# Performance work log

Hardware: AMD Instinct MI355X
Metric: run time of the kernel (lower is better)

The kernel has to match this reference:

```python
import jax, jax.numpy as jnp
import numpy as np

SEQ, BATCH, HID, NLAYERS = 2048, 16, 1024, 2


def setup_inputs() -> dict:
    key = jax.random.key(0)
    ks = jax.random.split(key, 3)
    scale = 1.0 / np.sqrt(HID)
    x = jax.random.normal(ks[0], (SEQ, BATCH, HID), dtype=jnp.float32)
    W0 = jax.random.normal(ks[1], (HID, 3 * HID), dtype=jnp.float32) * scale
    b0 = jnp.zeros((2 * HID,), dtype=jnp.float32)
    W1 = jax.random.normal(ks[2], (HID, 3 * HID), dtype=jnp.float32) * scale
    b1 = jnp.zeros((2 * HID,), dtype=jnp.float32)
    return {"x": x, "W0": W0, "b0": b0, "W1": W1, "b1": b1}


def _sru_layer(x, W, b):
    # x: [L, B, H]; W: [H, 3H]; b: [2H]
    L, B, H = x.shape
    U = jnp.einsum('lbd,dk->lbk', x, W)  # [L, B, 3H]
    x_tilde = U[..., :H]
    bf, br = b[:H], b[H:]
    f = jax.nn.sigmoid(U[..., H:2 * H] + bf)  # forget gate [L,B,H]
    r = jax.nn.sigmoid(U[..., 2 * H:] + br)   # reset gate  [L,B,H]

    def step(c_prev, inp):
        xt_t, f_t = inp
        c_t = f_t * c_prev + (1.0 - f_t) * xt_t
        return c_t, c_t

    c0 = jnp.zeros((B, H), dtype=x.dtype)
    _, cs = jax.lax.scan(step, c0, (x_tilde, f))  # cs: [L, B, H]
    h = r * cs + (1.0 - r) * x  # highway connection
    return h


def reference(x, W0, b0, W1, b1):
    h = _sru_layer(x, W0, b0)
    h = _sru_layer(h, W1, b1)
    return h[-1:]  # [1, B, H], matching `out[-1:]`
```

## Files before the change

kernel.cpp:

```cpp
#include <hip/hip_runtime.h>

#define SEQ    2048
#define BATCH  16
#define HID    1024
#define M_TOT  (SEQ*BATCH)
#define NCH    (BATCH*HID)
#define NCHUNK 64
#define TCHUNK (SEQ/NCHUNK)
#define NSEG   256

typedef __attribute__((ext_vector_type(8))) short          short8;
typedef __attribute__((ext_vector_type(8))) unsigned short ushort8_t;
typedef __attribute__((ext_vector_type(4))) float          floatx4;

__device__ __forceinline__ unsigned short f32_to_bf16(float f) {
  unsigned int u = __float_as_uint(f);
  u += 0x7FFFu + ((u >> 16) & 1u);
  return (unsigned short)(u >> 16);
}
__device__ __forceinline__ float bf16_to_f32(unsigned short h) {
  return __uint_as_float(((unsigned int)h) << 16);
}
__device__ __forceinline__ float sigmoidf_(float x) {
  return 1.f / (1.f + __expf(-x));
}


__device__ __forceinline__ void cast_swizzle_body(const float* __restrict__ src,
    unsigned short* __restrict__ dst, int mt, int kt, int t) {
  __shared__ unsigned short tile[4096];
  const int r = t >> 1, kh = (t & 1) * 16;
  const float* sp = src + (size_t)(mt * 128 + r) * 1024 + kt * 32 + kh;
  float4 v0 = *(const float4*)(sp + 0);
  float4 v1 = *(const float4*)(sp + 4);
  float4 v2 = *(const float4*)(sp + 8);
  float4 v3 = *(const float4*)(sp + 12);
  ushort8_t u0, u1;
  u0[0]=f32_to_bf16(v0.x); u0[1]=f32_to_bf16(v0.y); u0[2]=f32_to_bf16(v0.z); u0[3]=f32_to_bf16(v0.w);
  u0[4]=f32_to_bf16(v1.x); u0[5]=f32_to_bf16(v1.y); u0[6]=f32_to_bf16(v1.z); u0[7]=f32_to_bf16(v1.w);
  u1[0]=f32_to_bf16(v2.x); u1[1]=f32_to_bf16(v2.y); u1[2]=f32_to_bf16(v2.z); u1[3]=f32_to_bf16(v2.w);
  u1[4]=f32_to_bf16(v3.x); u1[5]=f32_to_bf16(v3.y); u1[6]=f32_to_bf16(v3.z); u1[7]=f32_to_bf16(v3.w);
  const int c = r >> 4, lr = r & 15, q0 = kh >> 3;
  const int unit0 = c * 64 + (q0 << 4) + lr;
  *(ushort8_t*)&tile[unit0 * 8]        = u0;
  *(ushort8_t*)&tile[(unit0 + 16) * 8] = u1;
  __syncthreads();
  const size_t base = ((size_t)mt * 32 + kt) * 4096;
  *(ushort8_t*)&dst[base + t * 16]     = *(const ushort8_t*)&tile[t * 16];
  *(ushort8_t*)&dst[base + t * 16 + 8] = *(const ushort8_t*)&tile[t * 16 + 8];
}

__device__ __forceinline__ void w_prep_body(const float* __restrict__ W,
    unsigned short* __restrict__ Wsw, int nt, int kt, int t) {
  __shared__ unsigned short tile[4096];
  const int kk = t >> 3, n0 = (t & 7) * 16;
  const float* sp = W + (size_t)(kt * 32 + kk) * 3072 + nt * 128 + n0;
  float v[16];
#pragma unroll
  for (int i = 0; i < 16; i += 4) {
    float4 f = *(const float4*)(sp + i);
    v[i] = f.x; v[i+1] = f.y; v[i+2] = f.z; v[i+3] = f.w;
  }
  const int cbase = (n0 >> 4) * 64 + ((kk >> 3) << 4);
#pragma unroll
  for (int j = 0; j < 16; j++)
    tile[(cbase + j) * 8 + (kk & 7)] = f32_to_bf16(v[j]);
  __syncthreads();
  const size_t base = ((size_t)nt * 32 + kt) * 4096;
  *(ushort8_t*)&Wsw[base + t * 16]     = *(const ushort8_t*)&tile[t * 16];
  *(ushort8_t*)&Wsw[base + t * 16 + 8] = *(const ushort8_t*)&tile[t * 16 + 8];
}

__global__ __launch_bounds__(256) void prep_all(const float* __restrict__ x,
    const float* __restrict__ W0, const float* __restrict__ W1,
    unsigned short* __restrict__ xsw, unsigned short* __restrict__ W0sw,
    unsigned short* __restrict__ W1sw) {
  const int id = blockIdx.x, t = threadIdx.x;
  if (id < 8192)        cast_swizzle_body(x, xsw, id >> 5, id & 31, t);
  else if (id < 8960)   w_prep_body(W0, W0sw, (id - 8192) >> 5, (id - 8192) & 31, t);
  else                  w_prep_body(W1, W1sw, (id - 8960) >> 5, (id - 8960) & 31, t);
}

__global__ __launch_bounds__(256, 2) void gemm_direct(
    const unsigned short* __restrict__ A, const unsigned short* __restrict__ B,
    unsigned short* __restrict__ Xt, unsigned short* __restrict__ Fo, unsigned short* __restrict__ Ro,
    const float* __restrict__ bias, int NBN2)
{
  const int tid = threadIdx.x;
  const int wave = tid >> 6, lane = tid & 63;
  const int wm = wave & 1, wn = wave >> 1;
  const int id = blockIdx.x;
  const int xcd = id & 7, slot = id >> 3;
  const int NB8 = NBN2 << 3;
  const int g = slot / NB8, rem = slot - g * NB8;
  const int bn = rem >> 3;
  const int bm = xcd * 32 + g * 8 + (rem & 7);

  const unsigned short* gA = A + (size_t)bm * 32 * 4096 + wm * 2048 + lane * 8;
  const unsigned short* gB = B + ((size_t)(bn * 2 + wn)) * 32 * 4096 + lane * 8;

  floatx4 acc[4][8];
#pragma unroll
  for (int i = 0; i < 4; i++)
#pragma unroll
    for (int j = 0; j < 8; j++)
#pragma unroll
      for (int r = 0; r < 4; r++) acc[i][j][r] = 0.f;

  short8 a0[4], b0[8], a1[4], b1[8];
  auto loadA = [&](short8* d, const unsigned short* p) {
#pragma unroll
    for (int i = 0; i < 4; i++) d[i] = *(const short8*)(p + i * 512);
  };
  auto loadB = [&](short8* d, const unsigned short* p) {
#pragma unroll
    for (int j = 0; j < 8; j++) d[j] = *(const short8*)(p + j * 512);
  };
  auto domfma = [&](short8* a, short8* b) {
#pragma unroll
    for (int i = 0; i < 4; i++)
#pragma unroll
      for (int j = 0; j < 8; j++)
        acc[i][j] = __builtin_amdgcn_mfma_f32_16x16x32_bf16(a[i], b[j], acc[i][j], 0, 0, 0);
  };

  loadA(a0, gA); loadB(b0, gB);
#pragma unroll 1
  for (int kt = 0; kt < 32; kt += 2) {
    loadA(a1, gA + 4096); loadB(b1, gB + 4096);
    domfma(a0, b0);
    gA += 8192; gB += 8192;
    if (kt + 2 < 32) { loadA(a0, gA); loadB(b0, gB); }
    domfma(a1, b1);
  }

  const int region = bn >> 2;
  const int lc = (bn & 3) * 256 + wn * 128 + (lane & 15);
  const int row0 = bm * 128 + wm * 64 + ((lane >> 4) << 2);
  if (region == 0) {
#pragma unroll
    for (int i = 0; i < 4; i++)
#pragma unroll
      for (int j = 0; j < 8; j++)
#pragma unroll
        for (int rg = 0; rg < 4; rg++)
          Xt[(size_t)(row0 + i * 16 + rg) * 1024 + lc + j * 16] = f32_to_bf16(acc[i][j][rg]);
  } else {
    unsigned short* O = (region == 1) ? Fo : Ro;
    const float* bp = bias + (region - 1) * 1024;
#pragma unroll
    for (int j = 0; j < 8; j++) {
      float bb = bp[lc + j * 16];
#pragma unroll
      for (int i = 0; i < 4; i++)
#pragma unroll
        for (int rg = 0; rg < 4; rg++) {
          float s = sigmoidf_(acc[i][j][rg] + bb);
          O[(size_t)(row0 + i * 16 + rg) * 1024 + lc + j * 16] = f32_to_bf16(s);
        }
    }
  }
}

__global__ __launch_bounds__(256, 2) void gemm2_scan(
    const unsigned short* __restrict__ A, const unsigned short* __restrict__ B,
    const float* __restrict__ bias, float* __restrict__ Pseg, float* __restrict__ Sseg)
{
  __shared__ float lps[2][64][4][4][2];
  const int tid = threadIdx.x;
  const int wave = tid >> 6, lane = tid & 63;
  const int wm = wave & 1, wn = wave >> 1;
  const int id = blockIdx.x;
  const int xcd = id & 7, slot = id >> 3;
  const int g = slot >> 6, rem = slot & 63;
  const int bn = rem >> 3;
  const int bm = xcd * 32 + g * 8 + (rem & 7);

  const unsigned short* gA  = A + (size_t)bm * 32 * 4096 + wm * 2048 + lane * 8;
  const unsigned short* gBx = B + (size_t)bn * 32 * 4096 + wn * 2048 + lane * 8;
  const unsigned short* gBf = B + (size_t)(8 + bn) * 32 * 4096 + wn * 2048 + lane * 8;

  floatx4 ax[4][4], af[4][4];
#pragma unroll
  for (int i = 0; i < 4; i++)
#pragma unroll
    for (int j = 0; j < 4; j++)
#pragma unroll
      for (int r = 0; r < 4; r++) { ax[i][j][r] = 0.f; af[i][j][r] = 0.f; }

  short8 a0[4], bx0[4], bf0[4], a1[4], bx1[4], bf1[4];
  auto load4 = [&](short8* d, const unsigned short* p) {
#pragma unroll
    for (int i = 0; i < 4; i++) d[i] = *(const short8*)(p + i * 512);
  };
  auto domfma = [&](short8* a, short8* bx, short8* bf) {
#pragma unroll
    for (int i = 0; i < 4; i++)
#pragma unroll
      for (int j = 0; j < 4; j++) {
        ax[i][j] = __builtin_amdgcn_mfma_f32_16x16x32_bf16(a[i], bx[j], ax[i][j], 0, 0, 0);
        af[i][j] = __builtin_amdgcn_mfma_f32_16x16x32_bf16(a[i], bf[j], af[i][j], 0, 0, 0);
      }
  };

  load4(a0, gA); load4(bx0, gBx); load4(bf0, gBf);
#pragma unroll 1
  for (int kt = 0; kt < 32; kt += 2) {
    load4(a1, gA + 4096); load4(bx1, gBx + 4096); load4(bf1, gBf + 4096);
    domfma(a0, bx0, bf0);
    gA += 8192; gBx += 8192; gBf += 8192;
    if (kt + 2 < 32) { load4(a0, gA); load4(bx0, gBx); load4(bf0, gBf); }
    domfma(a1, bx1, bf1);
  }

  const int q = lane >> 4, cc = lane & 15;
  float pv[4][4], sv[4][4];
#pragma unroll
  for (int j = 0; j < 4; j++) {
    float bb = bias[bn * 128 + wn * 64 + j * 16 + cc];
#pragma unroll
    for (int rg = 0; rg < 4; rg++) {
      float p = 1.f, s = 0.f;
#pragma unroll
      for (int i = 0; i < 4; i++) {
        float f  = sigmoidf_(af[i][j][rg] + bb);
        float xt = ax[i][j][rg];
        s = f * s + (1.f - f) * xt;
        p *= f;
      }
      pv[j][rg] = p; sv[j][rg] = s;
    }
  }
  if (wm == 0) {
#pragma unroll
    for (int j = 0; j < 4; j++)
#pragma unroll
      for (int rg = 0; rg < 4; rg++) {
        lps[wn][lane][rg][j][0] = pv[j][rg];
        lps[wn][lane][rg][j][1] = sv[j][rg];
      }
  }
  __syncthreads();
  if (wm == 1) {
#pragma unroll
    for (int j = 0; j < 4; j++) {
      const int h = bn * 128 + wn * 64 + j * 16 + cc;
#pragma unroll
      for (int rg = 0; rg < 4; rg++) {
        float plo = lps[wn][lane][rg][j][0];
        float slo = lps[wn][lane][rg][j][1];
        float phi = pv[j][rg], shi = sv[j][rg];
        const size_t off = (size_t)bm * NCH + (q * 4 + rg) * 1024 + h;
        Pseg[off] = plo * phi;
        Sseg[off] = phi * slo + shi;
      }
    }
  }
}

__global__ __launch_bounds__(256) void scan_pass1(
    const unsigned short* __restrict__ Xt, const unsigned short* __restrict__ F,
    float* __restrict__ P, float* __restrict__ S) {
  const int ch = (blockIdx.x * 256 + threadIdx.x) * 8;
  const int chunk = blockIdx.y;
  size_t idx = (size_t)chunk * TCHUNK * NCH + ch;
  float p[8], s[8];
#pragma unroll
  for (int j = 0; j < 8; j++) { p[j] = 1.f; s[j] = 0.f; }
  for (int t = 0; t < TCHUNK; ++t) {
    ushort8_t fv = *(const ushort8_t*)&F[idx];
    ushort8_t xv = *(const ushort8_t*)&Xt[idx];
#pragma unroll
    for (int j = 0; j < 8; j++) {
      float f  = bf16_to_f32(fv[j]);
      float xt = bf16_to_f32(xv[j]);
      s[j] = f * s[j] + (1.f - f) * xt;
      p[j] *= f;
    }
    idx += NCH;
  }
  float4* P4 = (float4*)&P[(size_t)chunk * NCH + ch];
  float4* S4 = (float4*)&S[(size_t)chunk * NCH + ch];
  P4[0] = make_float4(p[0], p[1], p[2], p[3]);
  P4[1] = make_float4(p[4], p[5], p[6], p[7]);
  S4[0] = make_float4(s[0], s[1], s[2], s[3]);
  S4[1] = make_float4(s[4], s[5], s[6], s[7]);
}

__global__ __launch_bounds__(256) void combine_c0(
    const float* __restrict__ P, const float* __restrict__ S, float* __restrict__ C0) {
  const int ch = blockIdx.x * 256 + threadIdx.x;
  float c = 0.f;
#pragma unroll 4
  for (int k = 0; k < NCHUNK; ++k) {
    C0[(size_t)k * NCH + ch] = c;
    c = P[(size_t)k * NCH + ch] * c + S[(size_t)k * NCH + ch];
  }
}

#define TPAD 4112
__global__ __launch_bounds__(256) void scan1_pass2_fused(
    const unsigned short* __restrict__ Xt, const unsigned short* __restrict__ F,
    const unsigned short* __restrict__ R, unsigned short* __restrict__ xsw,
    const float* __restrict__ C0, unsigned short* __restrict__ h1last)
{
  __shared__ unsigned short st[4 * TPAD];
  const int hb = blockIdx.x;
  const int chunk = blockIdx.y;
  const int tid = threadIdx.x;
  const int b = tid >> 4, hg = tid & 15;
  const int h0 = hb * 128 + hg * 8;
  const int ch = b * 1024 + h0;
  const int tl   = hg >> 2;
  const int usub = (hg & 3) * 16 + b;

  float c[8];
  {
    const float4* C4 = (const float4*)&C0[(size_t)chunk * NCH + ch];
    float4 a = C4[0], d = C4[1];
    c[0]=a.x; c[1]=a.y; c[2]=a.z; c[3]=a.w; c[4]=d.x; c[5]=d.y; c[6]=d.z; c[7]=d.w;
  }

  size_t idx = (size_t)chunk * TCHUNK * NCH + ch;
  for (int t8 = 0; t8 < TCHUNK / 8; ++t8) {
#pragma unroll
    for (int ts = 0; ts < 8; ++ts) {
      const int t = chunk * TCHUNK + t8 * 8 + ts;
      ushort8_t fv = *(const ushort8_t*)&F[idx];
      ushort8_t xv = *(const ushort8_t*)&Xt[idx];
      ushort8_t rv = *(const ushort8_t*)&R[idx];
      const size_t soff = ((size_t)(t >> 3) * 32 + (h0 >> 5)) * 4096
                        + (size_t)(((t & 7) * 64 + usub) * 8);
      ushort8_t xo = *(const ushort8_t*)&xsw[soff];
      ushort8_t hv;
#pragma unroll
      for (int j = 0; j < 8; ++j) {
        float f  = bf16_to_f32(fv[j]);
        float xt = bf16_to_f32(xv[j]);
        c[j] = f * c[j] + (1.f - f) * xt;
        float r  = bf16_to_f32(rv[j]);
        float xval = bf16_to_f32(xo[j]);
        hv[j] = f32_to_bf16(r * c[j] + (1.f - r) * xval);
      }
      *(ushort8_t*)&st[tl * TPAD + (ts * 64 + usub) * 8] = hv;
      if (t == SEQ - 1) *(ushort8_t*)&h1last[ch] = hv;
      idx += NCH;
    }
    __syncthreads();
    const size_t gbase = (((size_t)chunk * (TCHUNK / 8) + t8) * 32 + hb * 4) * 4096;
#pragma unroll
    for (int tl2 = 0; tl2 < 4; ++tl2) {
      size_t gdst = gbase + (size_t)tl2 * 4096 + tid * 16;
      *(ushort8_t*)&xsw[gdst]     = *(const ushort8_t*)&st[tl2 * TPAD + tid * 16];
      *(ushort8_t*)&xsw[gdst + 8] = *(const ushort8_t*)&st[tl2 * TPAD + tid * 16 + 8];
    }
    __syncthreads();
  }
}

__global__ __launch_bounds__(256) void r2_kernel(
    const unsigned short* __restrict__ h1last, const float* __restrict__ W1,
    const float* __restrict__ b1, float* __restrict__ r2) {
  __shared__ float xrow[1024];
  const int b = blockIdx.x, nq = blockIdx.y, tid = threadIdx.x;
  for (int i = tid; i < 1024; i += 256)
    xrow[i] = bf16_to_f32(h1last[b * 1024 + i]);
  __syncthreads();
  const int n = nq * 256 + tid;
  float acc = b1[1024 + n];
  for (int d = 0; d < 1024; ++d)
    acc += xrow[d] * W1[(size_t)d * 3072 + 2048 + n];
  r2[b * 1024 + n] = sigmoidf_(acc);
}

__global__ __launch_bounds__(256) void final_l2(
    const float* __restrict__ Pseg, const float* __restrict__ Sseg,
    const float* __restrict__ r2, const unsigned short* __restrict__ h1last,
    float* __restrict__ out) {
  const int ch = blockIdx.x * 256 + threadIdx.x;
  float c = 0.f;
#pragma unroll 8
  for (int k = 0; k < NSEG; ++k)
    c = Pseg[(size_t)k * NCH + ch] * c + Sseg[(size_t)k * NCH + ch];
  float r = r2[ch];
  float x = bf16_to_f32(h1last[ch]);
  out[ch] = r * c + (1.f - r) * x;
}

extern "C" void kernel_launch(void* const* d_in, const int* in_sizes, int n_in,
                              void* d_out, int out_size, void* d_ws, size_t ws_size,
                              hipStream_t stream) {
  const float* x  = (const float*)d_in[0];
  const float* W0 = (const float*)d_in[1];
  const float* b0 = (const float*)d_in[2];
  const float* W1 = (const float*)d_in[3];
  const float* b1 = (const float*)d_in[4];
  float* out = (float*)d_out;

  char* ws = (char*)d_ws;
  auto alloc = [&](size_t bytes) {
    char* p = ws; ws += (bytes + 255) & ~(size_t)255; return p;
  };
  const size_t NE = (size_t)M_TOT * HID;
  unsigned short* xsw   = (unsigned short*)alloc(NE * 2);
  unsigned short* W0sw  = (unsigned short*)alloc((size_t)3072 * 1024 * 2);
  unsigned short* W1sw  = (unsigned short*)alloc((size_t)3072 * 1024 * 2);
  unsigned short* Xt    = (unsigned short*)alloc(NE * 2);
  unsigned short* F     = (unsigned short*)alloc(NE * 2);
  unsigned short* R     = (unsigned short*)alloc(NE * 2);
  unsigned short* h1last= (unsigned short*)alloc((size_t)NCH * 2);
  float* P    = (float*)alloc((size_t)NCHUNK * NCH * 4);
  float* S    = (float*)alloc((size_t)NCHUNK * NCH * 4);
  float* C0   = (float*)alloc((size_t)NCHUNK * NCH * 4);
  float* Pseg = (float*)alloc((size_t)NSEG * NCH * 4);
  float* Sseg = (float*)alloc((size_t)NSEG * NCH * 4);
  float* r2   = (float*)alloc((size_t)NCH * 4);

  dim3 blk256(256);
  prep_all<<<dim3(9728), blk256, 0, stream>>>(x, W0, W1, xsw, W0sw, W1sw);
  gemm_direct<<<dim3(256 * 12), blk256, 0, stream>>>(xsw, W0sw, Xt, F, R, b0, 12);
  scan_pass1<<<dim3(8, NCHUNK), blk256, 0, stream>>>(Xt, F, P, S);
  combine_c0<<<dim3(NCH / 256), blk256, 0, stream>>>(P, S, C0);
  scan1_pass2_fused<<<dim3(8, NCHUNK), blk256, 0, stream>>>(Xt, F, R, xsw, C0, h1last);
  r2_kernel<<<dim3(16, 4), blk256, 0, stream>>>(h1last, W1, b1, r2);
  gemm2_scan<<<dim3(2048), blk256, 0, stream>>>(xsw, W1sw, b1, Pseg, Sseg);
  final_l2<<<dim3(NCH / 256), blk256, 0, stream>>>(Pseg, Sseg, r2, h1last, out);
}
```

Baseline: 757.9 us.

## Replace first-layer direct-load GEMM with LDS-staged 4-buffer pipelined GEMM

The first-layer projection GEMM used to feed MFMAs straight from global memory into registers. It now uses a 512-thread block computing a 256x256 tile. Operands are staged into a 4-slot LDS ring buffer via global_load_lds, and the A/B loads for stage t+3 are interleaved with the MFMA work of stage t, coordinated with barriers, setprio and partial vmcnt waits. This aims to raise reuse per loaded byte and hide global latency. The cost is 128KB of LDS per block, which limits residency to one block per CU, plus a more fragile hand-scheduled synchronisation scheme.

```diff
diff --git a/kernel.cpp b/kernel.cpp
--- a/kernel.cpp
+++ b/kernel.cpp
@@ -81,82 +81,157 @@
   else                  w_prep_body(W1, W1sw, (id - 8960) >> 5, (id - 8960) & 31, t);
 }
 
-__global__ __launch_bounds__(256, 2) void gemm_direct(
+typedef __attribute__((address_space(1))) const unsigned int GUI;
+typedef __attribute__((address_space(3))) unsigned int LUI;
+__device__ __forceinline__ void gl16(const unsigned short* g, unsigned short* l) {
+  __builtin_amdgcn_global_load_lds((GUI*)g, (LUI*)l, 16, 0, 0);
+}
+
+__global__ __launch_bounds__(512, 2) void gemm_pipe(
     const unsigned short* __restrict__ A, const unsigned short* __restrict__ B,
-    unsigned short* __restrict__ Xt, unsigned short* __restrict__ Fo, unsigned short* __restrict__ Ro,
-    const float* __restrict__ bias, int NBN2)
+    unsigned short* __restrict__ Xt, unsigned short* __restrict__ Fo,
+    unsigned short* __restrict__ Ro, const float* __restrict__ bias)
 {
+  __shared__ unsigned short lds[65536];
   const int tid = threadIdx.x;
   const int wave = tid >> 6, lane = tid & 63;
-  const int wm = wave & 1, wn = wave >> 1;
+  const int wm = wave >> 2, wn = wave & 3;
   const int id = blockIdx.x;
   const int xcd = id & 7, slot = id >> 3;
-  const int NB8 = NBN2 << 3;
-  const int g = slot / NB8, rem = slot - g * NB8;
-  const int bn = rem >> 3;
-  const int bm = xcd * 32 + g * 8 + (rem & 7);
-
-  const unsigned short* gA = A + (size_t)bm * 32 * 4096 + wm * 2048 + lane * 8;
-  const unsigned short* gB = B + ((size_t)(bn * 2 + wn)) * 32 * 4096 + lane * 8;
-
-  floatx4 acc[4][8];
-#pragma unroll
-  for (int i = 0; i < 4; i++)
-#pragma unroll
-    for (int j = 0; j < 8; j++)
-#pragma unroll
-      for (int r = 0; r < 4; r++) acc[i][j][r] = 0.f;
-
-  short8 a0[4], b0[8], a1[4], b1[8];
-  auto loadA = [&](short8* d, const unsigned short* p) {
-#pragma unroll
-    for (int i = 0; i < 4; i++) d[i] = *(const short8*)(p + i * 512);
-  };
-  auto loadB = [&](short8* d, const unsigned short* p) {
-#pragma unroll
-    for (int j = 0; j < 8; j++) d[j] = *(const short8*)(p + j * 512);
-  };
-  auto domfma = [&](short8* a, short8* b) {
-#pragma unroll
-    for (int i = 0; i < 4; i++)
-#pragma unroll
-      for (int j = 0; j < 8; j++)
-        acc[i][j] = __builtin_amdgcn_mfma_f32_16x16x32_bf16(a[i], b[j], acc[i][j], 0, 0, 0);
-  };
-
-  loadA(a0, gA); loadB(b0, gB);
+  const int g = slot / 96, r = slot % 96;
+  const int bn = r >> 3;
+  const int bm = xcd * 16 + g * 8 + (r & 7);
+
+  const unsigned short* aSrc0 = A + ((size_t)(2 * bm + 0) * 32) * 4096 + tid * 8;
+  const unsigned short* aSrc1 = A + ((size_t)(2 * bm + 1) * 32) * 4096 + tid * 8;
+  const unsigned short* bSrc0 = B + ((size_t)(2 * bn + 0) * 32) * 4096 + tid * 8;
+  const unsigned short* bSrc1 = B + ((size_t)(2 * bn + 1) * 32) * 4096 + tid * 8;
+
+  floatx4 acc[8][4];
+#pragma unroll
+  for (int i = 0; i < 8; i++)
+#pragma unroll
+    for (int j = 0; j < 4; j++)
+#pragma unroll
+      for (int rr = 0; rr < 4; rr++) acc[i][j][rr] = 0.f;
+
+#pragma unroll
+  for (int u = 0; u < 3; ++u) {
+    unsigned short* d = &lds[u * 16384 + wave * 512];
+    gl16(aSrc0 + (size_t)u * 4096, d);
+    gl16(aSrc1 + (size_t)u * 4096, d + 4096);
+    gl16(bSrc0 + (size_t)u * 4096, d + 8192);
+    gl16(bSrc1 + (size_t)u * 4096, d + 12288);
+  }
+  asm volatile("s_waitcnt vmcnt(0)" ::: "memory");
+  __builtin_amdgcn_s_barrier();
+
+  const int aoff = wm * 4096 + lane * 8;
+  const int boff = 8192 + (wn >> 1) * 4096 + (wn & 1) * 2048 + lane * 8;
+
 #pragma unroll 1
-  for (int kt = 0; kt < 32; kt += 2) {
-    loadA(a1, gA + 4096); loadB(b1, gB + 4096);
-    domfma(a0, b0);
-    gA += 8192; gB += 8192;
-    if (kt + 2 < 32) { loadA(a0, gA); loadB(b0, gB); }
-    domfma(a1, b1);
+  for (int t = 0; t < 29; ++t) {
+    __builtin_amdgcn_sched_barrier(0);
+    const int sb = (t & 3) * 16384;
+    const int u = t + 3;
+    const unsigned short* As = &lds[sb + aoff];
+    const unsigned short* Bs = &lds[sb + boff];
+    short8 br[4], ar[4];
+#pragma unroll
+    for (int nj = 0; nj < 4; ++nj) br[nj] = *(const short8*)(Bs + nj * 512);
+#pragma unroll
+    for (int mi = 0; mi < 4; ++mi) ar[mi] = *(const short8*)(As + mi * 512);
+    {
+      unsigned short* d = &lds[(u & 3) * 16384 + wave * 512];
+      gl16(aSrc0 + (size_t)u * 4096, d);
+      gl16(aSrc1 + (size_t)u * 4096, d + 4096);
+    }
+    __builtin_amdgcn_s_barrier();
+    __builtin_amdgcn_s_setprio(1);
+#pragma unroll
+    for (int mi = 0; mi < 4; ++mi)
+#pragma unroll
+      for (int nj = 0; nj < 4; ++nj)
+        acc[mi][nj] = __builtin_amdgcn_mfma_f32_16x16x32_bf16(ar[mi], br[nj], acc[mi][nj], 0, 0, 0);
+    __builtin_amdgcn_s_setprio(0);
+    __builtin_amdgcn_s_barrier();
+#pragma unroll
+    for (int mi = 0; mi < 4; ++mi) ar[mi] = *(const short8*)(As + (4 + mi) * 512);
+    {
+      unsigned short* d = &lds[(u & 3) * 16384 + 8192 + wave * 512];
+      gl16(bSrc0 + (size_t)u * 4096, d);
+      gl16(bSrc1 + (size_t)u * 4096, d + 4096);
+    }
+    __builtin_amdgcn_s_barrier();
+    __builtin_amdgcn_s_setprio(1);
+#pragma unroll
+    for (int mi = 0; mi < 4; ++mi)
+#pragma unroll
+      for (int nj = 0; nj < 4; ++nj)
+        acc[4 + mi][nj] = __builtin_amdgcn_mfma_f32_16x16x32_bf16(ar[mi], br[nj], acc[4 + mi][nj], 0, 0, 0);
+    __builtin_amdgcn_s_setprio(0);
+    asm volatile("s_waitcnt vmcnt(8)" ::: "memory");
+    __builtin_amdgcn_s_barrier();
+  }
+#pragma unroll 1
+  for (int t = 29; t < 32; ++t) {
+    __builtin_amdgcn_sched_barrier(0);
+    const int sb = (t & 3) * 16384;
+    const unsigned short* As = &lds[sb + aoff];
+    const unsigned short* Bs = &lds[sb + boff];
+    short8 br[4], ar[4];
+#pragma unroll
+    for (int nj = 0; nj < 4; ++nj) br[nj] = *(const short8*)(Bs + nj * 512);
+#pragma unroll
+    for (int mi = 0; mi < 4; ++mi) ar[mi] = *(const short8*)(As + mi * 512);
+    __builtin_amdgcn_s_barrier();
+    __builtin_amdgcn_s_setprio(1);
+#pragma unroll
+    for (int mi = 0; mi < 4; ++mi)
+#pragma unroll
+      for (int nj = 0; nj < 4; ++nj)
+        acc[mi][nj] = __builtin_amdgcn_mfma_f32_16x16x32_bf16(ar[mi], br[nj], acc[mi][nj], 0, 0, 0);
+    __builtin_amdgcn_s_setprio(0);
+    __builtin_amdgcn_s_barrier();
+#pragma unroll
+    for (int mi = 0; mi < 4; ++mi) ar[mi] = *(const short8*)(As + (4 + mi) * 512);
+    __builtin_amdgcn_s_barrier();
+    __builtin_amdgcn_s_setprio(1);
+#pragma unroll
+    for (int mi = 0; mi < 4; ++mi)
+#pragma unroll
+      for (int nj = 0; nj < 4; ++nj)
+        acc[4 + mi][nj] = __builtin_amdgcn_mfma_f32_16x16x32_bf16(ar[mi], br[nj], acc[4 + mi][nj], 0, 0, 0);
+    __builtin_amdgcn_s_setprio(0);
+    if (t < 31) asm volatile("s_waitcnt vmcnt(0)" ::: "memory");
+    __builtin_amdgcn_s_barrier();
   }
 
   const int region = bn >> 2;
-  const int lc = (bn & 3) * 256 + wn * 128 + (lane & 15);
-  const int row0 = bm * 128 + wm * 64 + ((lane >> 4) << 2);
+  const int cc = lane & 15, q = lane >> 4;
+  const int lc0 = (bn & 3) * 256 + wn * 64 + cc;
+  const int row0 = bm * 256 + wm * 128 + q * 4;
   if (region == 0) {
 #pragma unroll
-    for (int i = 0; i < 4; i++)
-#pragma unroll
-      for (int j = 0; j < 8; j++)
-#pragma unroll
-        for (int rg = 0; rg < 4; rg++)
-          Xt[(size_t)(row0 + i * 16 + rg) * 1024 + lc + j * 16] = f32_to_bf16(acc[i][j][rg]);
+    for (int mi = 0; mi < 8; ++mi)
+#pragma unroll
+      for (int nj = 0; nj < 4; ++nj)
+#pragma unroll
+        for (int rg = 0; rg < 4; ++rg)
+          Xt[(size_t)(row0 + mi * 16 + rg) * 1024 + lc0 + nj * 16] =
+              f32_to_bf16(acc[mi][nj][rg]);
   } else {
     unsigned short* O = (region == 1) ? Fo : Ro;
     const float* bp = bias + (region - 1) * 1024;
 #pragma unroll
-    for (int j = 0; j < 8; j++) {
-      float bb = bp[lc + j * 16];
-#pragma unroll
-      for (int i = 0; i < 4; i++)
-#pragma unroll
-        for (int rg = 0; rg < 4; rg++) {
-          float s = sigmoidf_(acc[i][j][rg] + bb);
-          O[(size_t)(row0 + i * 16 + rg) * 1024 + lc + j * 16] = f32_to_bf16(s);
+    for (int nj = 0; nj < 4; ++nj) {
+      float bb = bp[lc0 + nj * 16];
+#pragma unroll
+      for (int mi = 0; mi < 8; ++mi)
+#pragma unroll
+        for (int rg = 0; rg < 4; ++rg) {
+          float s = sigmoidf_(acc[mi][nj][rg] + bb);
+          O[(size_t)(row0 + mi * 16 + rg) * 1024 + lc0 + nj * 16] = f32_to_bf16(s);
         }
     }
   }
@@ -418,7 +493,7 @@
 
   dim3 blk256(256);
   prep_all<<<dim3(9728), blk256, 0, stream>>>(x, W0, W1, xsw, W0sw, W1sw);
-  gemm_direct<<<dim3(256 * 12), blk256, 0, stream>>>(xsw, W0sw, Xt, F, R, b0, 12);
+  gemm_pipe<<<dim3(1536), dim3(512), 0, stream>>>(xsw, W0sw, Xt, F, R, b0);
   scan_pass1<<<dim3(8, NCHUNK), blk256, 0, stream>>>(Xt, F, P, S);
   combine_c0<<<dim3(NCH / 256), blk256, 0, stream>>>(P, S, C0);
   scan1_pass2_fused<<<dim3(8, NCHUNK), blk256, 0, stream>>>(Xt, F, R, xsw, C0, h1last);
```

After: 767.9 us. Within noise of the previous version (+1.3%).
